# Kernel tuning notes

Hardware: AMD Instinct MI355X
Metric: run time of the kernel (lower is better)

Reference implementation:

```python
import jax, jax.numpy as jnp
import numpy as np

S, B, D = 2048, 2, 1024   # seq_len, batch, d_model
H, Dh = 16, 64            # n_head, d_head (H*Dh == D)
LN_EPS = 1e-5


def _rel_shift(x):
    # x: [qlen, klen, bsz, n_head] -- standard Transformer-XL relative shift
    q, k, b, n = x.shape
    x = jnp.pad(x, ((0, 0), (1, 0), (0, 0), (0, 0)))  # [q, k+1, b, n]
    x = x.reshape(k + 1, q, b, n)[1:]                  # drop first row
    return x.reshape(q, k, b, n)


def setup_inputs() -> dict:
    key = jax.random.key(0)
    ks = jax.random.split(key, 8)
    s = 0.02
    return {
        "x":    jax.random.normal(ks[0], (S, B, D), jnp.float32),
        "r":    jax.random.normal(ks[1], (1, D), jnp.float32),          # learned pos vector
        "rw":   jax.random.normal(ks[2], (H, Dh), jnp.float32),          # content bias
        "rr":   jax.random.normal(ks[3], (H, Dh), jnp.float32),          # position bias
        "ln_g": jnp.ones((D,), jnp.float32),
        "ln_b": jnp.zeros((D,), jnp.float32),
        "Wqkv": jax.random.normal(ks[4], (D, 3 * H * Dh), jnp.float32) * s,
        "Wr":   jax.random.normal(ks[5], (D, H * Dh), jnp.float32) * s,
        "Wo":   jax.random.normal(ks[6], (H * Dh, D), jnp.float32) * s,
    }


def reference(x, r, rw, rr, ln_g, ln_b, Wqkv, Wr, Wo):
    # Pre-LayerNorm (dropout = identity in eval mode)
    mu = jnp.mean(x, axis=-1, keepdims=True)
    var = jnp.mean(jnp.square(x - mu), axis=-1, keepdims=True)
    xn = (x - mu) * jax.lax.rsqrt(var + LN_EPS) * ln_g + ln_b   # [S,B,D]

    # relative position input: r expanded over seq
    r_exp = jnp.broadcast_to(r, (S, D))                          # [S,D]

    qkv = xn @ Wqkv                                              # [S,B,3*H*Dh]
    q, k, v = jnp.split(qkv, 3, axis=-1)
    q = q.reshape(S, B, H, Dh)
    k = k.reshape(S, B, H, Dh)
    v = v.reshape(S, B, H, Dh)
    rk = (r_exp @ Wr).reshape(S, H, Dh)                          # [S,H,Dh]

    scale = 1.0 / np.sqrt(Dh).astype(np.float32)
    AC = jnp.einsum('ibnd,jbnd->ijbn', q + rw, k)                # content term
    BD = jnp.einsum('ibnd,jnd->ijbn', q + rr, rk)                # position term
    BD = _rel_shift(BD)
    attn = jax.nn.softmax((AC + BD) * scale, axis=1)             # over key axis j

    av = jnp.einsum('ijbn,jbnd->ibnd', attn, v).reshape(S, B, H * Dh)
    return xn + av @ Wo                                          # residual w/ normed input
```

## Files before the change

### kernel.cpp

```cpp
#include <hip/hip_runtime.h>

typedef unsigned short u16;
typedef __attribute__((ext_vector_type(8))) __bf16 bf16x8;
typedef __attribute__((ext_vector_type(8))) u16 u16x8;
typedef __attribute__((ext_vector_type(2))) unsigned u32x2;
typedef __attribute__((ext_vector_type(4))) float f32x4;
typedef __attribute__((ext_vector_type(16))) float f32x16;

__device__ __forceinline__ float bf2f(u16 u){
  union { unsigned int i; float f; } v; v.i = ((unsigned int)u) << 16; return v.f;
}
__device__ __forceinline__ u16 f2bf(float f){
  union { float f; unsigned int u; } v; v.f = f;
  unsigned int u = v.u;
  u += 0x7FFFu + ((u >> 16) & 1u);
  return (u16)(u >> 16);
}
__device__ __forceinline__ unsigned fbits(float f){
  union { float f; unsigned u; } v; v.f = f; return v.u;
}
__device__ __forceinline__ void gld_lds16(const u16* g, u16* l){
  __builtin_amdgcn_global_load_lds((const __attribute__((address_space(1))) unsigned int*)g,
                                   (__attribute__((address_space(3))) unsigned int*)l, 16, 0, 0);
}

__global__ __launch_bounds__(256) void prep_k(const float* __restrict__ Wqkv, u16* __restrict__ wqkvT,
                                              const float* __restrict__ Wo, u16* __restrict__ woT,
                                              const float* __restrict__ r, const float* __restrict__ Wr,
                                              float* __restrict__ rk0,
                                              const float* __restrict__ x, const float* __restrict__ gw,
                                              const float* __restrict__ bw, u16* __restrict__ xnb){
  __shared__ float tile[32][33];
  __shared__ float red[8];
  const int tx = threadIdx.x, ty = threadIdx.y;
  const int t = ty * 32 + tx;
  if(blockIdx.x == 128){
    const int n = blockIdx.y * 32 + (t & 31);
    const int chunk = t >> 5;
    float acc = 0.f;
    const int d0 = chunk * 128;
    for(int d = d0; d < d0 + 128; ++d)
      acc += r[d] * Wr[(size_t)d * 1024 + n];
    tile[chunk][t & 31] = acc;
    __syncthreads();
    if(chunk == 0){
      float s = 0.f;
      #pragma unroll
      for(int c = 0; c < 8; ++c) s += tile[c][t & 31];
      rk0[n] = s;
    }
    return;
  }
  if(blockIdx.x >= 129){
    const int row = (blockIdx.x - 129) * 32 + blockIdx.y;
    const float* xr = x + (size_t)row * 1024;
    float4 xv = *reinterpret_cast<const float4*>(xr + t * 4);
    float s  = xv.x + xv.y + xv.z + xv.w;
    float s2 = xv.x*xv.x + xv.y*xv.y + xv.z*xv.z + xv.w*xv.w;
    #pragma unroll
    for(int m = 1; m <= 32; m <<= 1){ s += __shfl_xor(s, m, 64); s2 += __shfl_xor(s2, m, 64); }
    const int w = t >> 6, lane = t & 63;
    if(lane == 0){ red[w] = s; red[4 + w] = s2; }
    __syncthreads();
    float S1 = red[0] + red[1] + red[2] + red[3];
    float S2 = red[4] + red[5] + red[6] + red[7];
    float mu = S1 * (1.f/1024.f);
    float var = S2 * (1.f/1024.f) - mu * mu;
    float rstd = rsqrtf(var + 1e-5f);
    float4 gv = *reinterpret_cast<const float4*>(gw + t * 4);
    float4 bv = *reinterpret_cast<const float4*>(bw + t * 4);
    ushort4 o;
    o.x = f2bf((xv.x - mu) * rstd * gv.x + bv.x);
    o.y = f2bf((xv.y - mu) * rstd * gv.y + bv.y);
    o.z = f2bf((xv.z - mu) * rstd * gv.z + bv.z);
    o.w = f2bf((xv.w - mu) * rstd * gv.w + bv.w);
    *reinterpret_cast<ushort4*>(xnb + (size_t)row * 1024 + t * 4) = o;
    return;
  }
  const float* in; u16* out; int C, bxx;
  if(blockIdx.x < 96){ in = Wqkv; out = wqkvT; C = 3072; bxx = blockIdx.x; }
  else               { in = Wo;   out = woT;   C = 1024; bxx = blockIdx.x - 96; }
  const int bx = bxx * 32, by = blockIdx.y * 32;
  #pragma unroll
  for(int i = 0; i < 32; i += 8)
    tile[ty + i][tx] = in[(size_t)(by + ty + i) * C + bx + tx];
  __syncthreads();
  #pragma unroll
  for(int i = 0; i < 32; i += 8)
    out[(size_t)(bx + ty + i) * 1024 + by + tx] = f2bf(tile[tx][ty + i]);
}

__global__ __launch_bounds__(256) void gemm_qkv_k(const u16* __restrict__ A, const u16* __restrict__ BT,
                                                  u16* __restrict__ Cb, u16* __restrict__ vT){
  __shared__ u16 sA[2][128 * 32];
  __shared__ u16 sB[2][128 * 32];
  __shared__ u16 tl[128 * 66];
  const int t = threadIdx.x;
  const int row0 = blockIdx.y * 128, col0 = blockIdx.x * 128;
  const int w = t >> 6, lane = t & 63, g = lane >> 4, lq = lane & 15;
  const int wr = (w >> 1) * 64, wc = (w & 1) * 64;
  const int K = 1024;
  f32x4 zero4 = {0.f, 0.f, 0.f, 0.f};
  f32x4 acc[4][4];
  #pragma unroll
  for(int mi = 0; mi < 4; ++mi)
    #pragma unroll
    for(int ni = 0; ni < 4; ++ni) acc[mi][ni] = zero4;

  for(int kt = 0; kt < K; kt += 64){
    #pragma unroll
    for(int ks = 0; ks < 2; ++ks){
      const int kk = kt + ks * 32;
      gld_lds16(A  + (size_t)(row0 +      (t >> 2)) * K + kk + (t & 3) * 8, &sA[ks][w * 512]);
      gld_lds16(A  + (size_t)(row0 + 64 + (t >> 2)) * K + kk + (t & 3) * 8, &sA[ks][2048 + w * 512]);
      gld_lds16(BT + (size_t)(col0 +      (t >> 2)) * K + kk + (t & 3) * 8, &sB[ks][w * 512]);
      gld_lds16(BT + (size_t)(col0 + 64 + (t >> 2)) * K + kk + (t & 3) * 8, &sB[ks][2048 + w * 512]);
    }
    __syncthreads();
    #pragma unroll
    for(int ks = 0; ks < 2; ++ks){
      bf16x8 af[4];
      #pragma unroll
      for(int mi = 0; mi < 4; ++mi)
        af[mi] = *reinterpret_cast<const bf16x8*>(&sA[ks][(wr + mi * 16 + lq) * 32 + g * 8]);
      #pragma unroll
      for(int ni = 0; ni < 4; ++ni){
        bf16x8 bfr = *reinterpret_cast<const bf16x8*>(&sB[ks][(wc + ni * 16 + lq) * 32 + g * 8]);
        #pragma unroll
        for(int mi = 0; mi < 4; ++mi)
          acc[mi][ni] = __builtin_amdgcn_mfma_f32_16x16x32_bf16(af[mi], bfr, acc[mi][ni], 0, 0, 0);
      }
    }
    __syncthreads();
  }
  if(blockIdx.x < 16){
    #pragma unroll
    for(int mi = 0; mi < 4; ++mi)
      #pragma unroll
      for(int ni = 0; ni < 4; ++ni)
        #pragma unroll
        for(int rg = 0; rg < 4; ++rg){
          const int row = row0 + wr + mi * 16 + g * 4 + rg;
          const int col = col0 + wc + ni * 16 + lq;
          Cb[(size_t)row * 2048 + col] = f2bf(acc[mi][ni][rg]);
        }
  } else {
    const int cv0 = col0 - 2048;
    #pragma unroll
    for(int half = 0; half < 2; ++half){
      if((w & 1) == half){
        #pragma unroll
        for(int mi = 0; mi < 4; ++mi)
          #pragma unroll
          for(int ni = 0; ni < 4; ++ni)
            #pragma unroll
            for(int rg = 0; rg < 4; ++rg)
              tl[(wr + mi * 16 + g * 4 + rg) * 66 + ni * 16 + lq] = f2bf(acc[mi][ni][rg]);
      }
      __syncthreads();
      const int h = (cv0 >> 6) + half;
      const int b2 = w >> 1, dup = w & 1, d = lane;
      const int R = (b2 * 16 + h) * 64 + d;
      u16 tmp[32];
      #pragma unroll
      for(int e = 0; e < 32; ++e)
        tmp[e] = tl[((dup * 32 + e) * 2 + b2) * 66 + d];
      u16* op = vT + (size_t)R * 2048 + (row0 >> 1) + dup * 32;
      *reinterpret_cast<u16x8*>(op)      = *reinterpret_cast<u16x8*>(&tmp[0]);
      *reinterpret_cast<u16x8*>(op + 8)  = *reinterpret_cast<u16x8*>(&tmp[8]);
      *reinterpret_cast<u16x8*>(op + 16) = *reinterpret_cast<u16x8*>(&tmp[16]);
      *reinterpret_cast<u16x8*>(op + 24) = *reinterpret_cast<u16x8*>(&tmp[24]);
      __syncthreads();
    }
  }
}

__global__ __launch_bounds__(256) void gemm_out_k(const u16* __restrict__ A, const u16* __restrict__ BT,
                                                  const u16* __restrict__ res, float* __restrict__ Cf){
  __shared__ u16 sA[128 * 32];
  __shared__ u16 sB[64 * 32];
  const int t = threadIdx.x;
  const int row0 = blockIdx.y * 128, col0 = blockIdx.x * 64;
  const int w = t >> 6, lane = t & 63, g = lane >> 4, lq = lane & 15;
  const int wr = (w >> 1) * 64, wc = (w & 1) * 32;
  const int K = 1024, N = 1024;
  f32x4 zero4 = {0.f, 0.f, 0.f, 0.f};
  f32x4 acc[4][2];
  #pragma unroll
  for(int mi = 0; mi < 4; ++mi)
    #pragma unroll
    for(int ni = 0; ni < 2; ++ni) acc[mi][ni] = zero4;

  for(int kt = 0; kt < K; kt += 32){
    gld_lds16(A  + (size_t)(row0 +      (t >> 2)) * K + kt + (t & 3) * 8, &sA[w * 512]);
    gld_lds16(A  + (size_t)(row0 + 64 + (t >> 2)) * K + kt + (t & 3) * 8, &sA[2048 + w * 512]);
    gld_lds16(BT + (size_t)(col0 +      (t >> 2)) * K + kt + (t & 3) * 8, &sB[w * 512]);
    __syncthreads();
    bf16x8 af[4];
    #pragma unroll
    for(int mi = 0; mi < 4; ++mi)
      af[mi] = *reinterpret_cast<const bf16x8*>(&sA[(wr + mi * 16 + lq) * 32 + g * 8]);
    #pragma unroll
    for(int ni = 0; ni < 2; ++ni){
      bf16x8 bfr = *reinterpret_cast<const bf16x8*>(&sB[(wc + ni * 16 + lq) * 32 + g * 8]);
      #pragma unroll
      for(int mi = 0; mi < 4; ++mi)
        acc[mi][ni] = __builtin_amdgcn_mfma_f32_16x16x32_bf16(af[mi], bfr, acc[mi][ni], 0, 0, 0);
    }
    __syncthreads();
  }
  #pragma unroll
  for(int mi = 0; mi < 4; ++mi)
    #pragma unroll
    for(int ni = 0; ni < 2; ++ni)
      #pragma unroll
      for(int rg = 0; rg < 4; ++rg){
        const int row = row0 + wr + mi * 16 + g * 4 + rg;
        const int col = col0 + wc + ni * 16 + lq;
        Cf[(size_t)row * N + col] = acc[mi][ni][rg] + bf2f(res[(size_t)row * N + col]);
      }
}

__global__ __launch_bounds__(256) void attn_k(const u16* __restrict__ qk, const u16* __restrict__ vT,
                                              const float* __restrict__ rw, const float* __restrict__ rr,
                                              const float* __restrict__ rk0, u16* __restrict__ av){
  constexpr int S = 2048, ST = 74;
  __shared__ u16 ks[2][64 * ST];
  __shared__ u16 vs[2][64 * ST];
  const int t = threadIdx.x;
  const int i0 = blockIdx.x * 128;
  const int bh = blockIdx.y;
  const int b = bh >> 4, h = bh & 15;
  const int w = t >> 6, lane = t & 63, m = lane & 31, q5 = lane >> 5;
  const int iw0 = i0 + w * 32;
  const int i_lane = iw0 + m;
  const float SC = 0.125f * 1.4426950408889634f;

  bf16x8 qf[4];
  float ciL, cpL;
  {
    const bool hasnext = (i_lane + 1 < S);
    const u16* qp  = qk + (size_t)(i_lane * 2 + b) * 2048 + h * 64;
    const u16* qp2 = qk + (size_t)((hasnext ? i_lane + 1 : i_lane) * 2 + b) * 2048 + h * 64;
    const float* rwp = rw  + h * 64;
    const float* rrp = rr  + h * 64;
    const float* rkp = rk0 + h * 64;
    float cpart = 0.f, cppart = 0.f;
    #pragma unroll
    for(int kt = 0; kt < 4; ++kt){
      const int dbase = kt * 16 + q5 * 8;
      u16x8 qv  = *reinterpret_cast<const u16x8*>(qp  + dbase);
      u16x8 qv2 = *reinterpret_cast<const u16x8*>(qp2 + dbase);
      u16x8 a;
      #pragma unroll
      for(int e = 0; e < 8; ++e){
        const float qe  = bf2f(qv[e]);
        const float rke = rkp[dbase + e];
        const float rre = rrp[dbase + e];
        a[e] = f2bf((qe + rwp[dbase + e]) * SC);
        cpart  += (qe + rre) * rke;
        cppart += (bf2f(qv2[e]) + rre) * rke;
      }
      qf[kt] = *reinterpret_cast<bf16x8*>(&a);
    }
    cpart  += __shfl_xor(cpart, 32, 64);
    cppart += __shfl_xor(cppart, 32, 64);
    ciL = cpart * SC;
    cpL = hasnext ? cppart * SC : 0.0f;
  }

  union { u16 us[8]; bf16x8 bf; } onesu;
  #pragma unroll
  for(int e = 0; e < 8; ++e) onesu.us[e] = 0x3F80;
  const bf16x8 ones = onesu.bf;

  f32x16 acc0, acc1, accS, z16;
  #pragma unroll
  for(int e = 0; e < 16; ++e) z16[e] = 0.f;
  acc0 = z16; acc1 = z16; accS = z16;

  const int jr = t >> 2, c0 = (t & 3) * 16;
  {
    const u16* kp = qk + (size_t)(jr * 2 + b) * 2048 + 1024 + h * 64 + c0;
    *reinterpret_cast<u16x8*>(&ks[0][jr * ST + c0])     = *reinterpret_cast<const u16x8*>(kp);
    *reinterpret_cast<u16x8*>(&ks[0][jr * ST + c0 + 8]) = *reinterpret_cast<const u16x8*>(kp + 8);
    const u16* vp = vT + ((size_t)bh * 64 + jr) * 2048 + c0;
    *reinterpret_cast<u16x8*>(&vs[0][jr * ST + c0])     = *reinterpret_cast<const u16x8*>(vp);
    *reinterpret_cast<u16x8*>(&vs[0][jr * ST + c0 + 8]) = *reinterpret_cast<const u16x8*>(vp + 8);
  }
  __syncthreads();

  for(int n = 0; n < 32; ++n){
    const int p = n & 1;
    u16x8 k0, k1, v0, v1;
    const bool pre = (n + 1 < 32);
    if(pre){
      const int j0n = (n + 1) * 64;
      const u16* kp = qk + (size_t)((j0n + jr) * 2 + b) * 2048 + 1024 + h * 64 + c0;
      k0 = *reinterpret_cast<const u16x8*>(kp);
      k1 = *reinterpret_cast<const u16x8*>(kp + 8);
      const u16* vp = vT + ((size_t)bh * 64 + jr) * 2048 + j0n + c0;
      v0 = *reinterpret_cast<const u16x8*>(vp);
      v1 = *reinterpret_cast<const u16x8*>(vp + 8);
    }
    const int j0 = n * 64;
    bf16x8 pfrag[4];
    #pragma unroll
    for(int jt = 0; jt < 2; ++jt){
      const int tj0 = j0 + jt * 32;
      f32x16 s = z16;
      __builtin_amdgcn_s_setprio(1);
      #pragma unroll
      for(int kt = 0; kt < 4; ++kt){
        bf16x8 ka = *reinterpret_cast<const bf16x8*>(&ks[p][(jt * 32 + m) * ST + kt * 16 + q5 * 8]);
        s = __builtin_amdgcn_mfma_f32_32x32x16_bf16(ka, qf[kt], s, 0, 0, 0);
      }
      __builtin_amdgcn_s_setprio(0);
      float pv[16];
      if(tj0 + 31 <= iw0){
        #pragma unroll
        for(int r2 = 0; r2 < 16; ++r2) pv[r2] = __builtin_amdgcn_exp2f(s[r2] + ciL);
      } else if(tj0 >= iw0 + 33){
        #pragma unroll
        for(int r2 = 0; r2 < 16; ++r2) pv[r2] = __builtin_amdgcn_exp2f(s[r2] + cpL);
      } else {
        #pragma unroll
        for(int r2 = 0; r2 < 16; ++r2){
          const int j = tj0 + (r2 & 3) + 8 * (r2 >> 2) + 4 * q5;
          const float t1 = (j <= i_lane) ? ciL : cpL;
          const float bdL = (j == i_lane + 1) ? 0.0f : t1;
          pv[r2] = __builtin_amdgcn_exp2f(s[r2] + bdL);
        }
      }
      unsigned pk[8];
      #pragma unroll
      for(int q = 0; q < 8; ++q)
        pk[q] = __builtin_amdgcn_perm(fbits(pv[2 * q + 1]), fbits(pv[2 * q]), 0x07060302);
      union { unsigned u[4]; bf16x8 bf; } f0, f1;
#if __has_builtin(__builtin_amdgcn_permlane32_swap)
      u32x2 r0 = __builtin_amdgcn_permlane32_swap(pk[0], pk[2], false, false);
      u32x2 r1 = __builtin_amdgcn_permlane32_swap(pk[1], pk[3], false, false);
      u32x2 r2 = __builtin_amdgcn_permlane32_swap(pk[4], pk[6], false, false);
      u32x2 r3 = __builtin_amdgcn_permlane32_swap(pk[5], pk[7], false, false);
      f0.u[0] = r0[0]; f0.u[2] = r0[1];
      f0.u[1] = r1[0]; f0.u[3] = r1[1];
      f1.u[0] = r2[0]; f1.u[2] = r2[1];
      f1.u[1] = r3[0]; f1.u[3] = r3[1];
#else
      unsigned sAx = (q5 == 0) ? pk[2] : pk[0];
      unsigned sAy = (q5 == 0) ? pk[3] : pk[1];
      unsigned rAx = (unsigned)__shfl_xor((int)sAx, 32, 64);
      unsigned rAy = (unsigned)__shfl_xor((int)sAy, 32, 64);
      unsigned sBx = (q5 == 0) ? pk[6] : pk[4];
      unsigned sBy = (q5 == 0) ? pk[7] : pk[5];
      unsigned rBx = (unsigned)__shfl_xor((int)sBx, 32, 64);
      unsigned rBy = (unsigned)__shfl_xor((int)sBy, 32, 64);
      if(q5 == 0){
        f0.u[0] = pk[0]; f0.u[1] = pk[1]; f0.u[2] = rAx; f0.u[3] = rAy;
        f1.u[0] = pk[4]; f1.u[1] = pk[5]; f1.u[2] = rBx; f1.u[3] = rBy;
      } else {
        f0.u[0] = rAx; f0.u[1] = rAy; f0.u[2] = pk[2]; f0.u[3] = pk[3];
        f1.u[0] = rBx; f1.u[1] = rBy; f1.u[2] = pk[6]; f1.u[3] = pk[7];
      }
#endif
      pfrag[jt * 2 + 0] = f0.bf;
      pfrag[jt * 2 + 1] = f1.bf;
    }
    __builtin_amdgcn_s_setprio(1);
    #pragma unroll
    for(int kt = 0; kt < 4; ++kt){
      bf16x8 va0 = *reinterpret_cast<const bf16x8*>(&vs[p][(m) * ST + kt * 16 + q5 * 8]);
      acc0 = __builtin_amdgcn_mfma_f32_32x32x16_bf16(va0, pfrag[kt], acc0, 0, 0, 0);
      bf16x8 va1 = *reinterpret_cast<const bf16x8*>(&vs[p][(32 + m) * ST + kt * 16 + q5 * 8]);
      acc1 = __builtin_amdgcn_mfma_f32_32x32x16_bf16(va1, pfrag[kt], acc1, 0, 0, 0);
      accS = __builtin_amdgcn_mfma_f32_32x32x16_bf16(ones, pfrag[kt], accS, 0, 0, 0);
    }
    __builtin_amdgcn_s_setprio(0);
    if(pre){
      const int q2 = p ^ 1;
      *reinterpret_cast<u16x8*>(&ks[q2][jr * ST + c0])     = k0;
      *reinterpret_cast<u16x8*>(&ks[q2][jr * ST + c0 + 8]) = k1;
      *reinterpret_cast<u16x8*>(&vs[q2][jr * ST + c0])     = v0;
      *reinterpret_cast<u16x8*>(&vs[q2][jr * ST + c0 + 8]) = v1;
    }
    __syncthreads();
  }
  const float rinv = 1.0f / accS[0];
  u16* op = av + (size_t)(i_lane * 2 + b) * 1024 + h * 64;
  #pragma unroll
  for(int dt = 0; dt < 2; ++dt){
    const f32x16& A = dt ? acc1 : acc0;
    #pragma unroll
    for(int rq = 0; rq < 4; ++rq){
      ushort4 o;
      o.x = f2bf(A[rq * 4 + 0] * rinv);
      o.y = f2bf(A[rq * 4 + 1] * rinv);
      o.z = f2bf(A[rq * 4 + 2] * rinv);
      o.w = f2bf(A[rq * 4 + 3] * rinv);
      const int d0 = dt * 32 + 8 * rq + 4 * q5;
      *reinterpret_cast<ushort4*>(op + d0) = o;
    }
  }
}

extern "C" void kernel_launch(void* const* d_in, const int* in_sizes, int n_in,
                              void* d_out, int out_size, void* d_ws, size_t ws_size,
                              hipStream_t stream){
  (void)in_sizes; (void)n_in; (void)out_size; (void)ws_size;
  const float* x    = (const float*)d_in[0];
  const float* r    = (const float*)d_in[1];
  const float* rw   = (const float*)d_in[2];
  const float* rr   = (const float*)d_in[3];
  const float* ln_g = (const float*)d_in[4];
  const float* ln_b = (const float*)d_in[5];
  const float* Wqkv = (const float*)d_in[6];
  const float* Wr   = (const float*)d_in[7];
  const float* Wo   = (const float*)d_in[8];
  char* ws = (char*)d_ws;
  u16*   xnb   = (u16*)(ws + 0);
  u16*   qk    = (u16*)(ws + 8388608);
  u16*   av    = (u16*)(ws + 25165824);
  u16*   woT   = (u16*)(ws + 33554432);
  u16*   wqkvT = (u16*)(ws + 35651584);
  u16*   vT    = (u16*)(ws + 41943040);
  float* rk0   = (float*)(ws + 50331648);
  float* out   = (float*)d_out;

  prep_k<<<dim3(257, 32), dim3(32, 8), 0, stream>>>(Wqkv, wqkvT, Wo, woT, r, Wr, rk0,
                                                    x, ln_g, ln_b, xnb);
  gemm_qkv_k<<<dim3(24, 32), 256, 0, stream>>>(xnb, wqkvT, qk, vT);
  attn_k<<<dim3(16, 32), 256, 0, stream>>>(qk, vT, rw, rr, rk0, av);
  gemm_out_k<<<dim3(16, 32), 256, 0, stream>>>(av, woT, xnb, out);
}
```

Measured before the change: 223.1 us.

## Load K/V fragments directly from global in attention; widen output GEMM tiles

The attention kernel drops its shared-memory double buffers and barriers and loads K and V MFMA fragments straight from global memory into registers each iteration. It also replaces the ones-matrix MFMA used for the softmax row sum with a scalar register accumulation plus a cross-half shuffle, and sets an occupancy hint of 3 blocks. The output GEMM doubles its N tile to 128 and stages two K-slices per barrier, halving the grid and the number of syncs. Each wave now fetches K/V tiles redundantly through the caches instead of sharing them via LDS, and the wider GEMM tile uses more registers.

```diff
diff --git a/kernel.cpp b/kernel.cpp
--- a/kernel.cpp
+++ b/kernel.cpp
@@ -177,42 +177,50 @@
 
 __global__ __launch_bounds__(256) void gemm_out_k(const u16* __restrict__ A, const u16* __restrict__ BT,
                                                   const u16* __restrict__ res, float* __restrict__ Cf){
-  __shared__ u16 sA[128 * 32];
-  __shared__ u16 sB[64 * 32];
+  __shared__ u16 sA[2][128 * 32];
+  __shared__ u16 sB[2][128 * 32];
   const int t = threadIdx.x;
-  const int row0 = blockIdx.y * 128, col0 = blockIdx.x * 64;
+  const int row0 = blockIdx.y * 128, col0 = blockIdx.x * 128;
   const int w = t >> 6, lane = t & 63, g = lane >> 4, lq = lane & 15;
-  const int wr = (w >> 1) * 64, wc = (w & 1) * 32;
+  const int wr = (w >> 1) * 64, wc = (w & 1) * 64;
   const int K = 1024, N = 1024;
   f32x4 zero4 = {0.f, 0.f, 0.f, 0.f};
-  f32x4 acc[4][2];
+  f32x4 acc[4][4];
   #pragma unroll
   for(int mi = 0; mi < 4; ++mi)
     #pragma unroll
-    for(int ni = 0; ni < 2; ++ni) acc[mi][ni] = zero4;
-
-  for(int kt = 0; kt < K; kt += 32){
-    gld_lds16(A  + (size_t)(row0 +      (t >> 2)) * K + kt + (t & 3) * 8, &sA[w * 512]);
-    gld_lds16(A  + (size_t)(row0 + 64 + (t >> 2)) * K + kt + (t & 3) * 8, &sA[2048 + w * 512]);
-    gld_lds16(BT + (size_t)(col0 +      (t >> 2)) * K + kt + (t & 3) * 8, &sB[w * 512]);
-    __syncthreads();
-    bf16x8 af[4];
-    #pragma unroll
-    for(int mi = 0; mi < 4; ++mi)
-      af[mi] = *reinterpret_cast<const bf16x8*>(&sA[(wr + mi * 16 + lq) * 32 + g * 8]);
-    #pragma unroll
-    for(int ni = 0; ni < 2; ++ni){
-      bf16x8 bfr = *reinterpret_cast<const bf16x8*>(&sB[(wc + ni * 16 + lq) * 32 + g * 8]);
+    for(int ni = 0; ni < 4; ++ni) acc[mi][ni] = zero4;
+
+  for(int kt = 0; kt < K; kt += 64){
+    #pragma unroll
+    for(int ks = 0; ks < 2; ++ks){
+      const int kk = kt + ks * 32;
+      gld_lds16(A  + (size_t)(row0 +      (t >> 2)) * K + kk + (t & 3) * 8, &sA[ks][w * 512]);
+      gld_lds16(A  + (size_t)(row0 + 64 + (t >> 2)) * K + kk + (t & 3) * 8, &sA[ks][2048 + w * 512]);
+      gld_lds16(BT + (size_t)(col0 +      (t >> 2)) * K + kk + (t & 3) * 8, &sB[ks][w * 512]);
+      gld_lds16(BT + (size_t)(col0 + 64 + (t >> 2)) * K + kk + (t & 3) * 8, &sB[ks][2048 + w * 512]);
+    }
+    __syncthreads();
+    #pragma unroll
+    for(int ks = 0; ks < 2; ++ks){
+      bf16x8 af[4];
       #pragma unroll
       for(int mi = 0; mi < 4; ++mi)
-        acc[mi][ni] = __builtin_amdgcn_mfma_f32_16x16x32_bf16(af[mi], bfr, acc[mi][ni], 0, 0, 0);
+        af[mi] = *reinterpret_cast<const bf16x8*>(&sA[ks][(wr + mi * 16 + lq) * 32 + g * 8]);
+      #pragma unroll
+      for(int ni = 0; ni < 4; ++ni){
+        bf16x8 bfr = *reinterpret_cast<const bf16x8*>(&sB[ks][(wc + ni * 16 + lq) * 32 + g * 8]);
+        #pragma unroll
+        for(int mi = 0; mi < 4; ++mi)
+          acc[mi][ni] = __builtin_amdgcn_mfma_f32_16x16x32_bf16(af[mi], bfr, acc[mi][ni], 0, 0, 0);
+      }
     }
     __syncthreads();
   }
   #pragma unroll
   for(int mi = 0; mi < 4; ++mi)
     #pragma unroll
-    for(int ni = 0; ni < 2; ++ni)
+    for(int ni = 0; ni < 4; ++ni)
       #pragma unroll
       for(int rg = 0; rg < 4; ++rg){
         const int row = row0 + wr + mi * 16 + g * 4 + rg;
@@ -221,12 +229,10 @@
       }
 }
 
-__global__ __launch_bounds__(256) void attn_k(const u16* __restrict__ qk, const u16* __restrict__ vT,
-                                              const float* __restrict__ rw, const float* __restrict__ rr,
-                                              const float* __restrict__ rk0, u16* __restrict__ av){
-  constexpr int S = 2048, ST = 74;
-  __shared__ u16 ks[2][64 * ST];
-  __shared__ u16 vs[2][64 * ST];
+__global__ __launch_bounds__(256, 3) void attn_k(const u16* __restrict__ qk, const u16* __restrict__ vT,
+                                                 const float* __restrict__ rw, const float* __restrict__ rr,
+                                                 const float* __restrict__ rk0, u16* __restrict__ av){
+  constexpr int S = 2048;
   const int t = threadIdx.x;
   const int i0 = blockIdx.x * 128;
   const int bh = blockIdx.y;
@@ -269,41 +275,30 @@
     cpL = hasnext ? cppart * SC : 0.0f;
   }
 
-  union { u16 us[8]; bf16x8 bf; } onesu;
-  #pragma unroll
-  for(int e = 0; e < 8; ++e) onesu.us[e] = 0x3F80;
-  const bf16x8 ones = onesu.bf;
-
-  f32x16 acc0, acc1, accS, z16;
+  f32x16 acc0, acc1, z16;
   #pragma unroll
   for(int e = 0; e < 16; ++e) z16[e] = 0.f;
-  acc0 = z16; acc1 = z16; accS = z16;
-
-  const int jr = t >> 2, c0 = (t & 3) * 16;
-  {
-    const u16* kp = qk + (size_t)(jr * 2 + b) * 2048 + 1024 + h * 64 + c0;
-    *reinterpret_cast<u16x8*>(&ks[0][jr * ST + c0])     = *reinterpret_cast<const u16x8*>(kp);
-    *reinterpret_cast<u16x8*>(&ks[0][jr * ST + c0 + 8]) = *reinterpret_cast<const u16x8*>(kp + 8);
-    const u16* vp = vT + ((size_t)bh * 64 + jr) * 2048 + c0;
-    *reinterpret_cast<u16x8*>(&vs[0][jr * ST + c0])     = *reinterpret_cast<const u16x8*>(vp);
-    *reinterpret_cast<u16x8*>(&vs[0][jr * ST + c0 + 8]) = *reinterpret_cast<const u16x8*>(vp + 8);
-  }
-  __syncthreads();
+  acc0 = z16; acc1 = z16;
+  float rsum = 0.f;
+
+  const u16* kp0 = qk + (size_t)((m)      * 2 + b) * 2048 + 1024 + h * 64 + q5 * 8;
+  const u16* kp1 = qk + (size_t)((32 + m) * 2 + b) * 2048 + 1024 + h * 64 + q5 * 8;
+  const u16* vp0 = vT + ((size_t)bh * 64 + m)      * 2048 + q5 * 8;
+  const u16* vp1 = vT + ((size_t)bh * 64 + 32 + m) * 2048 + q5 * 8;
 
   for(int n = 0; n < 32; ++n){
-    const int p = n & 1;
-    u16x8 k0, k1, v0, v1;
-    const bool pre = (n + 1 < 32);
-    if(pre){
-      const int j0n = (n + 1) * 64;
-      const u16* kp = qk + (size_t)((j0n + jr) * 2 + b) * 2048 + 1024 + h * 64 + c0;
-      k0 = *reinterpret_cast<const u16x8*>(kp);
-      k1 = *reinterpret_cast<const u16x8*>(kp + 8);
-      const u16* vp = vT + ((size_t)bh * 64 + jr) * 2048 + j0n + c0;
-      v0 = *reinterpret_cast<const u16x8*>(vp);
-      v1 = *reinterpret_cast<const u16x8*>(vp + 8);
-    }
     const int j0 = n * 64;
+    bf16x8 ka0[4], ka1[4], vaA[4], vaB[4];
+    #pragma unroll
+    for(int kt = 0; kt < 4; ++kt){
+      ka0[kt] = *reinterpret_cast<const bf16x8*>(kp0 + kt * 16);
+      ka1[kt] = *reinterpret_cast<const bf16x8*>(kp1 + kt * 16);
+    }
+    #pragma unroll
+    for(int kt = 0; kt < 4; ++kt){
+      vaA[kt] = *reinterpret_cast<const bf16x8*>(vp0 + kt * 16);
+      vaB[kt] = *reinterpret_cast<const bf16x8*>(vp1 + kt * 16);
+    }
     bf16x8 pfrag[4];
     #pragma unroll
     for(int jt = 0; jt < 2; ++jt){
@@ -312,7 +307,7 @@
       __builtin_amdgcn_s_setprio(1);
       #pragma unroll
       for(int kt = 0; kt < 4; ++kt){
-        bf16x8 ka = *reinterpret_cast<const bf16x8*>(&ks[p][(jt * 32 + m) * ST + kt * 16 + q5 * 8]);
+        bf16x8 ka = jt ? ka1[kt] : ka0[kt];
         s = __builtin_amdgcn_mfma_f32_32x32x16_bf16(ka, qf[kt], s, 0, 0, 0);
       }
       __builtin_amdgcn_s_setprio(0);
@@ -332,6 +327,8 @@
           pv[r2] = __builtin_amdgcn_exp2f(s[r2] + bdL);
         }
       }
+      #pragma unroll
+      for(int r2 = 0; r2 < 16; ++r2) rsum += pv[r2];
       unsigned pk[8];
       #pragma unroll
       for(int q = 0; q < 8; ++q)
@@ -369,23 +366,17 @@
     __builtin_amdgcn_s_setprio(1);
     #pragma unroll
     for(int kt = 0; kt < 4; ++kt){
-      bf16x8 va0 = *reinterpret_cast<const bf16x8*>(&vs[p][(m) * ST + kt * 16 + q5 * 8]);
-      acc0 = __builtin_amdgcn_mfma_f32_32x32x16_bf16(va0, pfrag[kt], acc0, 0, 0, 0);
-      bf16x8 va1 = *reinterpret_cast<const bf16x8*>(&vs[p][(32 + m) * ST + kt * 16 + q5 * 8]);
-      acc1 = __builtin_amdgcn_mfma_f32_32x32x16_bf16(va1, pfrag[kt], acc1, 0, 0, 0);
-      accS = __builtin_amdgcn_mfma_f32_32x32x16_bf16(ones, pfrag[kt], accS, 0, 0, 0);
+      acc0 = __builtin_amdgcn_mfma_f32_32x32x16_bf16(vaA[kt], pfrag[kt], acc0, 0, 0, 0);
+      acc1 = __builtin_amdgcn_mfma_f32_32x32x16_bf16(vaB[kt], pfrag[kt], acc1, 0, 0, 0);
     }
     __builtin_amdgcn_s_setprio(0);
-    if(pre){
-      const int q2 = p ^ 1;
-      *reinterpret_cast<u16x8*>(&ks[q2][jr * ST + c0])     = k0;
-      *reinterpret_cast<u16x8*>(&ks[q2][jr * ST + c0 + 8]) = k1;
-      *reinterpret_cast<u16x8*>(&vs[q2][jr * ST + c0])     = v0;
-      *reinterpret_cast<u16x8*>(&vs[q2][jr * ST + c0 + 8]) = v1;
-    }
-    __syncthreads();
-  }
-  const float rinv = 1.0f / accS[0];
+    kp0 += 64 * 2 * 2048;
+    kp1 += 64 * 2 * 2048;
+    vp0 += 64;
+    vp1 += 64;
+  }
+  rsum += __shfl_xor(rsum, 32, 64);
+  const float rinv = 1.0f / rsum;
   u16* op = av + (size_t)(i_lane * 2 + b) * 1024 + h * 64;
   #pragma unroll
   for(int dt = 0; dt < 2; ++dt){
@@ -430,5 +421,5 @@
                                                     x, ln_g, ln_b, xnb);
   gemm_qkv_k<<<dim3(24, 32), 256, 0, stream>>>(xnb, wqkvT, qk, vT);
   attn_k<<<dim3(16, 32), 256, 0, stream>>>(qk, vT, rw, rr, rk0, av);
-  gemm_out_k<<<dim3(16, 32), 256, 0, stream>>>(av, woT, xnb, out);
-}
+  gemm_out_k<<<dim3(8, 32), 256, 0, stream>>>(av, woT, xnb, out);
+}
```

Result: slower. 298.5 us (+33.8%).
